# Optimization experiments

Measured on AMD Instinct MI355X. Metric: run time of the kernel, lower is better.

The kernel has to match this reference:

```python
import jax, jax.numpy as jnp
import numpy as np

N, F = 8192, 1024


def _lin_params(key, out_f, in_f):
    kw, kb = jax.random.split(key)
    w = jax.random.normal(kw, (out_f, in_f), dtype=jnp.float32) * 0.02
    b = jax.random.normal(kb, (out_f,), dtype=jnp.float32) * 0.02
    return w, b


def setup_inputs() -> dict:
    key = jax.random.key(0)
    ks = jax.random.split(key, 11)
    X = jax.random.normal(ks[0], (N, F), dtype=jnp.float32)
    A = jax.random.uniform(ks[1], (N, N), dtype=jnp.float32)
    W1_w, W1_b = _lin_params(ks[2], 512, F)
    t1_w, t1_b = _lin_params(ks[3], 1, 512)
    r1_w, r1_b = _lin_params(ks[4], 1, 512)
    W2_w, W2_b = _lin_params(ks[5], 256, 512)
    t2_w, t2_b = _lin_params(ks[6], 1, 256)
    r2_w, r2_b = _lin_params(ks[7], 1, 256)
    W3_w, W3_b = _lin_params(ks[8], 64, 256)
    t3_w, t3_b = _lin_params(ks[9], 1, 64)
    r3_w, r3_b = _lin_params(ks[10], 1, 64)
    return dict(X=X, A=A,
                W1_w=W1_w, W1_b=W1_b, t1_w=t1_w, t1_b=t1_b, r1_w=r1_w, r1_b=r1_b,
                W2_w=W2_w, W2_b=W2_b, t2_w=t2_w, t2_b=t2_b, r2_w=r2_w, r2_b=r2_b,
                W3_w=W3_w, W3_b=W3_b, t3_w=t3_w, t3_b=t3_b, r3_w=r3_w, r3_b=r3_b)


def _gat_layer(H, A, W_w, W_b, t_w, t_b, r_w, r_b):
    Z = jax.nn.relu(H @ W_w.T + W_b)                     # [N, out]
    t = (Z @ t_w.T + t_b)[:, 0]                          # [N] = vkt(Z)
    r = (Z @ r_w.T + r_b)[:, 0]                          # [N] = vkr(Z)
    # M_s = A * vkt(Z).T  -> M_s[i,j] = A[i,j] * t[j]
    # M_r = (A * vkr(Z).T).T -> M_r[i,j] = A[j,i] * r[i]
    M = A * t[None, :] + A.T * r[:, None]
    att = jax.nn.softmax(jax.nn.sigmoid(M), axis=1)      # torch default dim=1 for 2D
    return att @ Z


def reference(X, A,
              W1_w, W1_b, t1_w, t1_b, r1_w, r1_b,
              W2_w, W2_b, t2_w, t2_b, r2_w, r2_b,
              W3_w, W3_b, t3_w, t3_b, r3_w, r3_b):
    H1 = _gat_layer(X, A, W1_w, W1_b, t1_w, t1_b, r1_w, r1_b)
    H2 = _gat_layer(H1, A, W2_w, W2_b, t2_w, t2_b, r2_w, r2_b)
    H3 = _gat_layer(H2, A, W3_w, W3_b, t3_w, t3_b, r3_w, r3_b)
    return H3
```

## Files before the change

kernel.cpp:

```cpp
#include <hip/hip_runtime.h>
#include <math.h>

#define NN 8192

typedef __attribute__((ext_vector_type(8))) short short8;
typedef __attribute__((ext_vector_type(4))) float f32x4;

__device__ __forceinline__ float bf2f(unsigned short u) {
    unsigned int x = ((unsigned int)u) << 16;
    return __builtin_bit_cast(float, x);
}
__device__ __forceinline__ unsigned short f2bf(float f) {
    unsigned int x = __builtin_bit_cast(unsigned int, f);
    x = x + 0x7FFFu + ((x >> 16) & 1u);
    return (unsigned short)(x >> 16);
}
__device__ __forceinline__ float fast_sigexp(float x) {
    float s = __builtin_amdgcn_rcpf(1.0f + __expf(-x));
    return __expf(s);
}
__device__ __forceinline__ void gload16(const void* g, void* l) {
    __builtin_amdgcn_global_load_lds(
        (const __attribute__((address_space(1))) unsigned int*)g,
        (__attribute__((address_space(3))) unsigned int*)l, 16, 0, 0);
}

__global__ __launch_bounds__(256) void cvt_bf16(
    const float* __restrict__ src, unsigned short* __restrict__ dst)
{
    size_t idx = ((size_t)blockIdx.x * 256 + threadIdx.x) * 8;
    float4 a = *(const float4*)(src + idx);
    float4 b = *(const float4*)(src + idx + 4);
    unsigned int w0 = (unsigned int)f2bf(a.x) | ((unsigned int)f2bf(a.y) << 16);
    unsigned int w1 = (unsigned int)f2bf(a.z) | ((unsigned int)f2bf(a.w) << 16);
    unsigned int w2 = (unsigned int)f2bf(b.x) | ((unsigned int)f2bf(b.y) << 16);
    unsigned int w3 = (unsigned int)f2bf(b.z) | ((unsigned int)f2bf(b.w) << 16);
    uint4 o = {w0, w1, w2, w3};
    *(uint4*)(dst + idx) = o;
}

template<typename AT> struct ALoad;
template<> struct ALoad<float> {
    static __device__ __forceinline__ void ld16(const float* p, float* d) {
        float4 v0 = ((const float4*)p)[0];
        float4 v1 = ((const float4*)p)[1];
        float4 v2 = ((const float4*)p)[2];
        float4 v3 = ((const float4*)p)[3];
        d[0]=v0.x; d[1]=v0.y; d[2]=v0.z; d[3]=v0.w;
        d[4]=v1.x; d[5]=v1.y; d[6]=v1.z; d[7]=v1.w;
        d[8]=v2.x; d[9]=v2.y; d[10]=v2.z; d[11]=v2.w;
        d[12]=v3.x; d[13]=v3.y; d[14]=v3.z; d[15]=v3.w;
    }
};
template<> struct ALoad<unsigned short> {
    static __device__ __forceinline__ void ld16(const unsigned short* p, float* d) {
        uint4 u0 = ((const uint4*)p)[0];
        uint4 u1 = ((const uint4*)p)[1];
        unsigned int wd[8] = {u0.x, u0.y, u0.z, u0.w, u1.x, u1.y, u1.z, u1.w};
        #pragma unroll
        for (int k = 0; k < 8; ++k) {
            d[2*k]   = __builtin_bit_cast(float, wd[k] << 16);
            d[2*k+1] = __builtin_bit_cast(float, wd[k] & 0xFFFF0000u);
        }
    }
};
template<typename AT> struct Stage16;
template<> struct Stage16<unsigned short> {
    static __device__ __forceinline__ void st(const unsigned short* g, unsigned short* l) {
        uint4 a = ((const uint4*)g)[0];
        uint4 b = ((const uint4*)g)[1];
        ((uint4*)l)[0] = a;
        ((uint4*)l)[1] = b;
    }
};
template<> struct Stage16<float> {
    static __device__ __forceinline__ void st(const float* g, unsigned short* l) {
        float v[16];
        ALoad<float>::ld16(g, v);
        unsigned int wd[8];
        #pragma unroll
        for (int k = 0; k < 8; ++k)
            wd[k] = (unsigned int)f2bf(v[2*k]) | ((unsigned int)f2bf(v[2*k+1]) << 16);
        uint4 s0 = {wd[0], wd[1], wd[2], wd[3]};
        uint4 s1 = {wd[4], wd[5], wd[6], wd[7]};
        ((uint4*)l)[0] = s0;
        ((uint4*)l)[1] = s1;
    }
};

__global__ __launch_bounds__(256) void proj_mfma(
    const unsigned short* __restrict__ Hbf,
    const unsigned short* __restrict__ Wbf,
    const float* __restrict__ bias,
    unsigned short* __restrict__ Zt,
    int K, int O)
{
    constexpr int MT = 4, NT = 2;
    __shared__ unsigned short smem[8704];
    unsigned short* As = smem;
    unsigned short* Bs = smem + 4096;
    const int tid = threadIdx.x;
    const int w = tid >> 6;
    const int lane = tid & 63;
    const int quad = lane >> 4;
    const int m16 = lane & 15;
    const int i0 = blockIdx.y * 128;
    const int o0 = blockIdx.x * 64;
    const int wm = w & 1;
    const int wn = w >> 1;

    const char* gpa[2]; void* lpa[2];
    #pragma unroll
    for (int n = 0; n < 2; ++n) {
        int o16 = n * 256 + w * 64 + lane;
        int row = o16 >> 2, ch = o16 & 3;
        int sc = ch ^ ((row >> 1) & 3);
        gpa[n] = (const char*)(Hbf + (size_t)(i0 + row) * K) + sc * 16;
        lpa[n] = (char*)As + n * 4096 + w * 1024 + lane * 16;
    }
    const char* gpb; void* lpb;
    {
        int o16 = w * 64 + lane;
        int row = o16 >> 2, ch = o16 & 3;
        int sc = ch ^ ((row >> 1) & 3);
        gpb = (const char*)(Wbf + (size_t)(o0 + row) * K) + sc * 16;
        lpb = (char*)Bs + w * 1024 + lane * 16;
    }
    int aoff[MT], boff[NT];
    #pragma unroll
    for (int mt = 0; mt < MT; ++mt) {
        int row = wm * 64 + mt * 16 + m16;
        int sc = quad ^ ((row >> 1) & 3);
        aoff[mt] = row * 32 + sc * 8;
    }
    #pragma unroll
    for (int nt = 0; nt < NT; ++nt) {
        int row = wn * 32 + nt * 16 + m16;
        int sc = quad ^ ((row >> 1) & 3);
        boff[nt] = row * 32 + sc * 8;
    }
    f32x4 acc[MT][NT];
    #pragma unroll
    for (int mt = 0; mt < MT; ++mt)
        #pragma unroll
        for (int nt = 0; nt < NT; ++nt)
            acc[mt][nt] = (f32x4){0.f, 0.f, 0.f, 0.f};

    for (int k0 = 0; k0 < K; k0 += 32) {
        gload16(gpa[0], lpa[0]); gpa[0] += 64;
        gload16(gpa[1], lpa[1]); gpa[1] += 64;
        gload16(gpb, lpb); gpb += 64;
        __syncthreads();
        short8 af[MT], bf_[NT];
        #pragma unroll
        for (int mt = 0; mt < MT; ++mt) af[mt] = *(const short8*)(As + aoff[mt]);
        #pragma unroll
        for (int nt = 0; nt < NT; ++nt) bf_[nt] = *(const short8*)(Bs + boff[nt]);
        #pragma unroll
        for (int mt = 0; mt < MT; ++mt)
            #pragma unroll
            for (int nt = 0; nt < NT; ++nt)
                acc[mt][nt] = __builtin_amdgcn_mfma_f32_16x16x32_bf16(
                    af[mt], bf_[nt], acc[mt][nt], 0, 0, 0);
        __syncthreads();
    }
    #pragma unroll
    for (int nt = 0; nt < NT; ++nt) {
        int ol = wn * 32 + nt * 16 + m16;
        float bv = bias[o0 + ol];
        #pragma unroll
        for (int mt = 0; mt < MT; ++mt)
            #pragma unroll
            for (int rg = 0; rg < 4; ++rg) {
                int il = wm * 64 + mt * 16 + quad * 4 + rg;
                smem[ol * 136 + il] = f2bf(fmaxf(acc[mt][nt][rg] + bv, 0.f));
            }
    }
    __syncthreads();
    #pragma unroll
    for (int c = 0; c < 4; ++c) {
        int cc = c * 256 + tid;
        int ol = cc >> 4;
        int ic = (cc & 15) << 3;
        *(uint4*)(Zt + (size_t)(o0 + ol) * NN + i0 + ic) = *(const uint4*)&smem[ol * 136 + ic];
    }
}

__global__ __launch_bounds__(256) void tr_zt(
    const unsigned short* __restrict__ Zt,
    const float* __restrict__ tw, const float* __restrict__ tb,
    const float* __restrict__ rw, const float* __restrict__ rb,
    float* __restrict__ t, float* __restrict__ r)
{
    const int i  = blockIdx.x * 256 + threadIdx.x;
    const int c0 = blockIdx.y * 64;
    float at = 0.f, ar = 0.f;
    for (int c = c0; c < c0 + 64; ++c) {
        float z = bf2f(Zt[(size_t)c * NN + i]);
        at = fmaf(z, tw[c], at);
        ar = fmaf(z, rw[c], ar);
    }
    if (blockIdx.y == 0) { at += tb[0]; ar += rb[0]; }
    atomicAdd(t + i, at);
    atomicAdd(r + i, ar);
}

template<int BN, typename AT>
__global__ __launch_bounds__(256) void attn_fused(
    const AT* __restrict__ A,
    const unsigned short* __restrict__ Zt,
    const float* __restrict__ t, const float* __restrict__ r,
    float* __restrict__ Hacc, float* __restrict__ denom,
    int O, int kcount)
{
    constexpr int BM = 128, BK = 32;
    constexpr int MT = 4;
    constexpr int NT = BN / 32;
    constexpr int NB = (BN * BK * 2) / 4096;
    __shared__ unsigned short As[BM * BK];
    __shared__ unsigned short Bs[2][BN * BK];
    __shared__ unsigned short Ac[BK][136];
    const int tid  = threadIdx.x;
    const int w    = tid >> 6;
    const int lane = tid & 63;
    const int quad = lane >> 4;
    const int m16  = lane & 15;
    const int i0 = blockIdx.y * BM;
    const int c0 = blockIdx.x * BN;
    const int wm = w & 1;
    const int wn = w >> 1;
    const int jbase = blockIdx.z * kcount * BK;

    const int ci = tid >> 1;
    const int jh = tid & 1;
    const float ri = r[i0 + ci];
    const int si = (ci >> 1) & 3;
    unsigned short* asw0 = As + ci * 32 + (((jh * 2)    ) ^ si) * 8;
    unsigned short* asw1 = As + ci * 32 + (((jh * 2) + 1) ^ si) * 8;
    const int sj = tid >> 3;
    const int sm = tid & 7;
    unsigned short* acw = &Ac[sj][sm * 16];

    const char* gpb[NB]; unsigned int lob[NB];
    #pragma unroll
    for (int n = 0; n < NB; ++n) {
        int o16 = n * 256 + w * 64 + lane;
        int row = o16 >> 2, ch = o16 & 3;
        int sc = ch ^ ((row >> 1) & 3);
        gpb[n] = (const char*)Zt + ((size_t)(c0 + row) * NN + jbase) * 2 + sc * 16;
        lob[n] = n * 4096 + w * 1024 + lane * 16;
    }
    int aoff[MT], boff[NT];
    #pragma unroll
    for (int mt = 0; mt < MT; ++mt) {
        int row = wm * 64 + mt * 16 + m16;
        int sc = quad ^ ((row >> 1) & 3);
        aoff[mt] = row * 32 + sc * 8;
    }
    #pragma unroll
    for (int nt = 0; nt < NT; ++nt) {
        int row = wn * (BN / 2) + nt * 16 + m16;
        int sc = quad ^ ((row >> 1) & 3);
        boff[nt] = row * 32 + sc * 8;
    }

    f32x4 acc[MT][NT];
    #pragma unroll
    for (int mt = 0; mt < MT; ++mt)
        #pragma unroll
        for (int nt = 0; nt < NT; ++nt)
            acc[mt][nt] = (f32x4){0.f, 0.f, 0.f, 0.f};

    #pragma unroll
    for (int n = 0; n < NB; ++n)
        gload16(gpb[n], (char*)Bs[0] + lob[n]);

    float rsum = 0.f;
    const AT* arow = A + (size_t)(i0 + ci) * NN + jbase + jh * 16;
    const float* tptr = t + jbase + jh * 16;

    for (int kk = 0; kk < kcount; ++kk) {
        const int j0 = jbase + kk * BK;
        if (kk + 1 < kcount) {
            #pragma unroll
            for (int n = 0; n < NB; ++n)
                gload16(gpb[n] + (size_t)(kk + 1) * 64, (char*)Bs[(kk + 1) & 1] + lob[n]);
        }
        Stage16<AT>::st(A + (size_t)(j0 + sj) * NN + i0 + sm * 16, acw);
        float av[16], tv[16];
        ALoad<AT>::ld16(arow + (size_t)kk * BK, av);
        ALoad<float>::ld16(tptr + kk * BK, tv);
        __syncthreads();
        unsigned int wd[8];
        #pragma unroll
        for (int e = 0; e < 16; ++e) {
            float aji = bf2f(Ac[jh * 16 + e][ci]);
            float x = fmaf(av[e], tv[e], aji * ri);
            float p = fast_sigexp(x);
            rsum += p;
            if (e & 1) wd[e >> 1] |= ((unsigned int)f2bf(p)) << 16;
            else       wd[e >> 1]  = (unsigned int)f2bf(p);
        }
        {
            uint4 s0 = {wd[0], wd[1], wd[2], wd[3]};
            uint4 s1 = {wd[4], wd[5], wd[6], wd[7]};
            *(uint4*)asw0 = s0;
            *(uint4*)asw1 = s1;
        }
        __syncthreads();
        const unsigned short* bsb = Bs[kk & 1];
        short8 af[MT], bf_[NT];
        #pragma unroll
        for (int mt = 0; mt < MT; ++mt) af[mt] = *(const short8*)(As + aoff[mt]);
        #pragma unroll
        for (int nt = 0; nt < NT; ++nt) bf_[nt] = *(const short8*)(bsb + boff[nt]);
        #pragma unroll
        for (int mt = 0; mt < MT; ++mt)
            #pragma unroll
            for (int nt = 0; nt < NT; ++nt)
                acc[mt][nt] = __builtin_amdgcn_mfma_f32_16x16x32_bf16(
                    af[mt], bf_[nt], acc[mt][nt], 0, 0, 0);
        __syncthreads();
    }

    rsum += __shfl_xor(rsum, 1);
    if (jh == 0 && blockIdx.x == 0)
        atomicAdd(denom + i0 + ci, rsum);

    const int colb = c0 + wn * (BN / 2) + m16;
    #pragma unroll
    for (int mt = 0; mt < MT; ++mt) {
        int rowb = i0 + wm * 64 + mt * 16 + quad * 4;
        #pragma unroll
        for (int rg = 0; rg < 4; ++rg) {
            float* orow = Hacc + (size_t)(rowb + rg) * O + colb;
            #pragma unroll
            for (int nt = 0; nt < NT; ++nt)
                atomicAdd(orow + nt * 16, acc[mt][nt][rg]);
        }
    }
}

__global__ __launch_bounds__(256) void norm_cvt(
    const float* __restrict__ Hacc, const float* __restrict__ denom,
    float* __restrict__ outf, unsigned short* __restrict__ outb, int O)
{
    const int gid = blockIdx.x * 256 + threadIdx.x;
    const int n4 = O >> 2;
    const int i = gid / n4;
    const int c = (gid % n4) << 2;
    float inv = __builtin_amdgcn_rcpf(denom[i]);
    float4 v = *(const float4*)(Hacc + (size_t)i * O + c);
    v.x *= inv; v.y *= inv; v.z *= inv; v.w *= inv;
    if (outf) {
        *(float4*)(outf + (size_t)i * O + c) = v;
    } else {
        ushort4 h;
        h.x = f2bf(v.x); h.y = f2bf(v.y); h.z = f2bf(v.z); h.w = f2bf(v.w);
        *(ushort4*)(outb + (size_t)i * O + c) = h;
    }
}

extern "C" void kernel_launch(void* const* d_in, const int* in_sizes, int n_in,
                              void* d_out, int out_size, void* d_ws, size_t ws_size,
                              hipStream_t stream)
{
    (void)in_sizes; (void)n_in; (void)out_size;
    const float* X = (const float*)d_in[0];
    const float* A = (const float*)d_in[1];
    const float* Wws[3] = {(const float*)d_in[2],  (const float*)d_in[8],  (const float*)d_in[14]};
    const float* Wbs[3] = {(const float*)d_in[3],  (const float*)d_in[9],  (const float*)d_in[15]};
    const float* tws[3] = {(const float*)d_in[4],  (const float*)d_in[10], (const float*)d_in[16]};
    const float* tbs[3] = {(const float*)d_in[5],  (const float*)d_in[11], (const float*)d_in[17]};
    const float* rws[3] = {(const float*)d_in[6],  (const float*)d_in[12], (const float*)d_in[18]};
    const float* rbs[3] = {(const float*)d_in[7],  (const float*)d_in[13], (const float*)d_in[19]};
    const int Ks[3] = {1024, 512, 256};
    const int Os[3] = {512, 256, 64};
    const int Zs[3] = {4, 8, 16};
    float* out = (float*)d_out;
    char* ws = (char*)d_ws;
    const size_t MB = (size_t)1 << 20;

    unsigned short* HbfX = (unsigned short*)(ws);
    unsigned short* Hbf2 = (unsigned short*)(ws + 16 * MB);
    unsigned short* Zt   = (unsigned short*)(ws + 24 * MB);
    float*          Hacc = (float*)(ws + 32 * MB);
    unsigned short* Wbf  = (unsigned short*)(ws + 48 * MB);
    float* tv = (float*)(ws + 50 * MB);
    float* rv = tv + NN;
    float* dv = rv + NN;
    unsigned short* Abf = (unsigned short*)(ws + 51 * MB);
    const bool useAbf = (ws_size >= 180 * MB);

    unsigned short* WbfL[3] = {Wbf, Wbf + 512 * 1024, Wbf + 512 * 1024 + 256 * 512};

    cvt_bf16<<<(NN * 1024) / 2048, 256, 0, stream>>>(X, HbfX);
    for (int L = 0; L < 3; ++L)
        cvt_bf16<<<(Os[L] * Ks[L]) / 2048, 256, 0, stream>>>(Wws[L], WbfL[L]);
    if (useAbf)
        cvt_bf16<<<(int)(((size_t)NN * NN) / 2048), 256, 0, stream>>>(A, Abf);

    const unsigned short* Hbf_in = HbfX;
    for (int L = 0; L < 3; ++L) {
        int K = Ks[L], O = Os[L];
        int zs = Zs[L];
        int kcount = NN / (zs * 32);
        proj_mfma<<<dim3(O / 64, NN / 128), 256, 0, stream>>>(
            Hbf_in, WbfL[L], Wbs[L], Zt, K, O);
        hipMemsetAsync(tv, 0, 96 * 1024, stream);
        tr_zt<<<dim3(NN / 256, O / 64), 256, 0, stream>>>(
            Zt, tws[L], tbs[L], rws[L], rbs[L], tv, rv);
        hipMemsetAsync(Hacc, 0, (size_t)NN * O * sizeof(float), stream);
        dim3 grid(O >= 128 ? O / 128 : 1, NN / 128, zs);
        if (useAbf) {
            if (O >= 128)
                attn_fused<128, unsigned short><<<grid, 256, 0, stream>>>(
                    Abf, Zt, tv, rv, Hacc, dv, O, kcount);
            else
                attn_fused<64, unsigned short><<<grid, 256, 0, stream>>>(
                    Abf, Zt, tv, rv, Hacc, dv, O, kcount);
        } else {
            if (O >= 128)
                attn_fused<128, float><<<grid, 256, 0, stream>>>(
                    A, Zt, tv, rv, Hacc, dv, O, kcount);
            else
                attn_fused<64, float><<<grid, 256, 0, stream>>>(
                    A, Zt, tv, rv, Hacc, dv, O, kcount);
        }
        float* outf = (L == 2) ? out : nullptr;
        unsigned short* outb = (L == 2) ? nullptr : Hbf2;
        norm_cvt<<<(NN / 256) * (O / 4), 256, 0, stream>>>(Hacc, dv, outf, outb, O);
        Hbf_in = Hbf2;
    }
}
```

Before: 1.002 ms.

## Widen attention column tile, prefetch next A/t tiles into registers, retune split-K

The fused attention kernel now uses a 256-wide output-column tile when O is at least 256. This cuts how many times each A element's sigmoid-exp is recomputed across column blocks. The main loop becomes software-pipelined: the next A row tile, the transposed A stage and the t values are loaded into registers or LDS after the MFMAs, instead of before the barrier. The Ac LDS buffer padding changes from 136 to 130 columns to reduce bank conflicts, and split-K factors rise for the first two layers to keep the grid filled. The wider tile doubles the accumulator registers, and the extra prefetch registers may reduce occupancy.

```diff
diff --git a/kernel.cpp b/kernel.cpp
--- a/kernel.cpp
+++ b/kernel.cpp
@@ -39,24 +39,14 @@
     *(uint4*)(dst + idx) = o;
 }
 
-template<typename AT> struct ALoad;
-template<> struct ALoad<float> {
-    static __device__ __forceinline__ void ld16(const float* p, float* d) {
-        float4 v0 = ((const float4*)p)[0];
-        float4 v1 = ((const float4*)p)[1];
-        float4 v2 = ((const float4*)p)[2];
-        float4 v3 = ((const float4*)p)[3];
-        d[0]=v0.x; d[1]=v0.y; d[2]=v0.z; d[3]=v0.w;
-        d[4]=v1.x; d[5]=v1.y; d[6]=v1.z; d[7]=v1.w;
-        d[8]=v2.x; d[9]=v2.y; d[10]=v2.z; d[11]=v2.w;
-        d[12]=v3.x; d[13]=v3.y; d[14]=v3.z; d[15]=v3.w;
-    }
-};
-template<> struct ALoad<unsigned short> {
-    static __device__ __forceinline__ void ld16(const unsigned short* p, float* d) {
-        uint4 u0 = ((const uint4*)p)[0];
-        uint4 u1 = ((const uint4*)p)[1];
-        unsigned int wd[8] = {u0.x, u0.y, u0.z, u0.w, u1.x, u1.y, u1.z, u1.w};
+template<typename AT> struct ARow;
+template<> struct ARow<unsigned short> {
+    struct Raw { uint4 a, b; };
+    static __device__ __forceinline__ Raw ld(const unsigned short* p) {
+        Raw r; r.a = ((const uint4*)p)[0]; r.b = ((const uint4*)p)[1]; return r;
+    }
+    static __device__ __forceinline__ void cvt(const Raw& r, float* d) {
+        unsigned int wd[8] = {r.a.x, r.a.y, r.a.z, r.a.w, r.b.x, r.b.y, r.b.z, r.b.w};
         #pragma unroll
         for (int k = 0; k < 8; ++k) {
             d[2*k]   = __builtin_bit_cast(float, wd[k] << 16);
@@ -64,27 +54,41 @@
         }
     }
 };
-template<typename AT> struct Stage16;
-template<> struct Stage16<unsigned short> {
+template<> struct ARow<float> {
+    struct Raw { float4 v[4]; };
+    static __device__ __forceinline__ Raw ld(const float* p) {
+        Raw r;
+        r.v[0] = ((const float4*)p)[0]; r.v[1] = ((const float4*)p)[1];
+        r.v[2] = ((const float4*)p)[2]; r.v[3] = ((const float4*)p)[3];
+        return r;
+    }
+    static __device__ __forceinline__ void cvt(const Raw& r, float* d) {
+        #pragma unroll
+        for (int q = 0; q < 4; ++q) {
+            d[4*q+0] = r.v[q].x; d[4*q+1] = r.v[q].y;
+            d[4*q+2] = r.v[q].z; d[4*q+3] = r.v[q].w;
+        }
+    }
+};
+template<typename AT> struct StageAc;
+template<> struct StageAc<unsigned short> {
     static __device__ __forceinline__ void st(const unsigned short* g, unsigned short* l) {
         uint4 a = ((const uint4*)g)[0];
         uint4 b = ((const uint4*)g)[1];
-        ((uint4*)l)[0] = a;
-        ((uint4*)l)[1] = b;
+        unsigned int* d = (unsigned int*)l;
+        d[0]=a.x; d[1]=a.y; d[2]=a.z; d[3]=a.w;
+        d[4]=b.x; d[5]=b.y; d[6]=b.z; d[7]=b.w;
     }
 };
-template<> struct Stage16<float> {
+template<> struct StageAc<float> {
     static __device__ __forceinline__ void st(const float* g, unsigned short* l) {
+        typename ARow<float>::Raw r = ARow<float>::ld(g);
         float v[16];
-        ALoad<float>::ld16(g, v);
-        unsigned int wd[8];
+        ARow<float>::cvt(r, v);
+        unsigned int* d = (unsigned int*)l;
         #pragma unroll
         for (int k = 0; k < 8; ++k)
-            wd[k] = (unsigned int)f2bf(v[2*k]) | ((unsigned int)f2bf(v[2*k+1]) << 16);
-        uint4 s0 = {wd[0], wd[1], wd[2], wd[3]};
-        uint4 s1 = {wd[4], wd[5], wd[6], wd[7]};
-        ((uint4*)l)[0] = s0;
-        ((uint4*)l)[1] = s1;
+            d[k] = (unsigned int)f2bf(v[2*k]) | ((unsigned int)f2bf(v[2*k+1]) << 16);
     }
 };
 
@@ -217,9 +221,10 @@
     constexpr int MT = 4;
     constexpr int NT = BN / 32;
     constexpr int NB = (BN * BK * 2) / 4096;
+    constexpr int BNK = BN * BK;
     __shared__ unsigned short As[BM * BK];
-    __shared__ unsigned short Bs[2][BN * BK];
-    __shared__ unsigned short Ac[BK][136];
+    __shared__ unsigned short Bs[2][BNK];
+    __shared__ unsigned short Ac[BK * 130];
     const int tid  = threadIdx.x;
     const int w    = tid >> 6;
     const int lane = tid & 63;
@@ -239,7 +244,8 @@
     unsigned short* asw1 = As + ci * 32 + (((jh * 2) + 1) ^ si) * 8;
     const int sj = tid >> 3;
     const int sm = tid & 7;
-    unsigned short* acw = &Ac[sj][sm * 16];
+    unsigned short* acw = Ac + sj * 130 + sm * 16;
+    const AT* astage = A + (size_t)(jbase + sj) * NN + i0 + sm * 16;
 
     const char* gpb[NB]; unsigned int lob[NB];
     #pragma unroll
@@ -271,31 +277,34 @@
         for (int nt = 0; nt < NT; ++nt)
             acc[mt][nt] = (f32x4){0.f, 0.f, 0.f, 0.f};
 
+    const AT* arow = A + (size_t)(i0 + ci) * NN + jbase + jh * 16;
+    const float* tptr = t + jbase + jh * 16;
+
     #pragma unroll
     for (int n = 0; n < NB; ++n)
         gload16(gpb[n], (char*)Bs[0] + lob[n]);
+    StageAc<AT>::st(astage, acw);
+    typename ARow<AT>::Raw avr = ARow<AT>::ld(arow);
+    float4 tvr0 = ((const float4*)tptr)[0];
+    float4 tvr1 = ((const float4*)tptr)[1];
+    float4 tvr2 = ((const float4*)tptr)[2];
+    float4 tvr3 = ((const float4*)tptr)[3];
+    __syncthreads();
 
     float rsum = 0.f;
-    const AT* arow = A + (size_t)(i0 + ci) * NN + jbase + jh * 16;
-    const float* tptr = t + jbase + jh * 16;
-
     for (int kk = 0; kk < kcount; ++kk) {
-        const int j0 = jbase + kk * BK;
-        if (kk + 1 < kcount) {
-            #pragma unroll
-            for (int n = 0; n < NB; ++n)
-                gload16(gpb[n] + (size_t)(kk + 1) * 64, (char*)Bs[(kk + 1) & 1] + lob[n]);
-        }
-        Stage16<AT>::st(A + (size_t)(j0 + sj) * NN + i0 + sm * 16, acw);
-        float av[16], tv[16];
-        ALoad<AT>::ld16(arow + (size_t)kk * BK, av);
-        ALoad<float>::ld16(tptr + kk * BK, tv);
-        __syncthreads();
+        const int b = kk & 1;
+        float av[16], tvv[16];
+        ARow<AT>::cvt(avr, av);
+        tvv[0]=tvr0.x; tvv[1]=tvr0.y; tvv[2]=tvr0.z; tvv[3]=tvr0.w;
+        tvv[4]=tvr1.x; tvv[5]=tvr1.y; tvv[6]=tvr1.z; tvv[7]=tvr1.w;
+        tvv[8]=tvr2.x; tvv[9]=tvr2.y; tvv[10]=tvr2.z; tvv[11]=tvr2.w;
+        tvv[12]=tvr3.x; tvv[13]=tvr3.y; tvv[14]=tvr3.z; tvv[15]=tvr3.w;
         unsigned int wd[8];
         #pragma unroll
         for (int e = 0; e < 16; ++e) {
-            float aji = bf2f(Ac[jh * 16 + e][ci]);
-            float x = fmaf(av[e], tv[e], aji * ri);
+            float aji = bf2f(Ac[(jh * 16 + e) * 130 + ci]);
+            float x = fmaf(av[e], tvv[e], aji * ri);
             float p = fast_sigexp(x);
             rsum += p;
             if (e & 1) wd[e >> 1] |= ((unsigned int)f2bf(p)) << 16;
@@ -308,18 +317,32 @@
             *(uint4*)asw1 = s1;
         }
         __syncthreads();
-        const unsigned short* bsb = Bs[kk & 1];
-        short8 af[MT], bf_[NT];
-        #pragma unroll
-        for (int mt = 0; mt < MT; ++mt) af[mt] = *(const short8*)(As + aoff[mt]);
-        #pragma unroll
-        for (int nt = 0; nt < NT; ++nt) bf_[nt] = *(const short8*)(bsb + boff[nt]);
-        #pragma unroll
-        for (int mt = 0; mt < MT; ++mt)
-            #pragma unroll
-            for (int nt = 0; nt < NT; ++nt)
-                acc[mt][nt] = __builtin_amdgcn_mfma_f32_16x16x32_bf16(
-                    af[mt], bf_[nt], acc[mt][nt], 0, 0, 0);
+        {
+            const unsigned short* bsb = Bs[b];
+            short8 af[MT], bf_[NT];
+            #pragma unroll
+            for (int mt = 0; mt < MT; ++mt) af[mt] = *(const short8*)(As + aoff[mt]);
+            #pragma unroll
+            for (int nt = 0; nt < NT; ++nt) bf_[nt] = *(const short8*)(bsb + boff[nt]);
+            #pragma unroll
+            for (int mt = 0; mt < MT; ++mt)
+                #pragma unroll
+                for (int nt = 0; nt < NT; ++nt)
+                    acc[mt][nt] = __builtin_amdgcn_mfma_f32_16x16x32_bf16(
+                        af[mt], bf_[nt], acc[mt][nt], 0, 0, 0);
+        }
+        if (kk + 1 < kcount) {
+            #pragma unroll
+            for (int n = 0; n < NB; ++n)
+                gload16(gpb[n] + (size_t)(kk + 1) * 64, (char*)Bs[b ^ 1] + lob[n]);
+            StageAc<AT>::st(astage + (size_t)(kk + 1) * BK * NN, acw);
+            avr = ARow<AT>::ld(arow + (size_t)(kk + 1) * BK);
+            const float* tp = tptr + (kk + 1) * BK;
+            tvr0 = ((const float4*)tp)[0];
+            tvr1 = ((const float4*)tp)[1];
+            tvr2 = ((const float4*)tp)[2];
+            tvr3 = ((const float4*)tp)[3];
+        }
         __syncthreads();
     }
 
@@ -376,7 +399,7 @@
     const float* rbs[3] = {(const float*)d_in[7],  (const float*)d_in[13], (const float*)d_in[19]};
     const int Ks[3] = {1024, 512, 256};
     const int Os[3] = {512, 256, 64};
-    const int Zs[3] = {4, 8, 16};
+    const int Zs[3] = {8, 16, 16};
     float* out = (float*)d_out;
     char* ws = (char*)d_ws;
     const size_t MB = (size_t)1 << 20;
@@ -411,17 +434,18 @@
         tr_zt<<<dim3(NN / 256, O / 64), 256, 0, stream>>>(
             Zt, tws[L], tbs[L], rws[L], rbs[L], tv, rv);
         hipMemsetAsync(Hacc, 0, (size_t)NN * O * sizeof(float), stream);
-        dim3 grid(O >= 128 ? O / 128 : 1, NN / 128, zs);
+        int gx = (O >= 256) ? O / 256 : 1;
+        dim3 grid(gx, NN / 128, zs);
         if (useAbf) {
-            if (O >= 128)
-                attn_fused<128, unsigned short><<<grid, 256, 0, stream>>>(
+            if (O >= 256)
+                attn_fused<256, unsigned short><<<grid, 256, 0, stream>>>(
                     Abf, Zt, tv, rv, Hacc, dv, O, kcount);
             else
                 attn_fused<64, unsigned short><<<grid, 256, 0, stream>>>(
                     Abf, Zt, tv, rv, Hacc, dv, O, kcount);
         } else {
-            if (O >= 128)
-                attn_fused<128, float><<<grid, 256, 0, stream>>>(
+            if (O >= 256)
+                attn_fused<256, float><<<grid, 256, 0, stream>>>(
                     A, Zt, tv, rv, Hacc, dv, O, kcount);
             else
                 attn_fused<64, float><<<grid, 256, 0, stream>>>(
```

Measured after the change: 954.0 us. 4.8% less time.
